# Optimization experiments

Measured on AMD Instinct MI355X. Metric: run time of the kernel, lower is better.

## Reference

```python
import jax, jax.numpy as jnp
import numpy as np

SCORE_THRESHOLD = 0.05
IOU_THRESHOLD = 0.5
MAX_DETECTIONS = 300
NEG = -1e9  # sentinel for suppressed / below-threshold scores


def setup_inputs() -> dict:
    key = jax.random.key(0)
    k1, k2, k3, k4 = jax.random.split(key, 4)
    B, N, C = 8, 49104, 20
    # valid corner-format boxes [x1, y1, x2, y2] inside a 512x512 image
    ctr = jax.random.uniform(k1, (B, N, 2), minval=0.0, maxval=512.0)
    wh = jax.random.uniform(k2, (B, N, 2), minval=8.0, maxval=128.0)
    boxes = jnp.concatenate([ctr - wh / 2, ctr + wh / 2], axis=-1)
    boxes3D = jax.random.normal(k3, (B, N, 16), dtype=jnp.float32)
    classification = jax.random.uniform(k4, (B, N, C)) ** 2
    return {"boxes": boxes, "boxes3D": boxes3D, "classification": classification}


def _iou_one_vs_all(box, boxes, areas):
    # box [4], boxes [N,4], areas [N] -> iou [N]
    lt = jnp.maximum(box[:2], boxes[:, :2])
    rb = jnp.minimum(box[2:], boxes[:, 2:])
    wh = jnp.maximum(rb - lt, 0.0)
    inter = wh[:, 0] * wh[:, 1]
    area = (box[2] - box[0]) * (box[3] - box[1])
    return inter / (areas + area - inter + 1e-9)


def _nms_class(boxes, areas, scores):
    # greedy NMS for one class; fixed MAX_DETECTIONS iterations (jit-friendly)
    s0 = jnp.where(scores > SCORE_THRESHOLD, scores, NEG)
    n = scores.shape[0]
    arange_n = jnp.arange(n)

    def step(s, _):
        i = jnp.argmax(s)
        valid = s[i] > NEG / 2
        iou = _iou_one_vs_all(boxes[i], boxes, areas)
        sup = (iou > IOU_THRESHOLD) | (arange_n == i)
        s_new = jnp.where(valid & sup, NEG, s)
        return s_new, (i, jnp.where(valid, s[i], NEG))

    _, (idx, sel) = jax.lax.scan(step, s0, None, length=MAX_DETECTIONS)
    return idx, sel  # [MAX_DETECTIONS] each


def _filter_image(boxes, boxes3D, cls):
    # boxes [N,4], boxes3D [N,16], cls [N,C]
    areas = (boxes[:, 2] - boxes[:, 0]) * (boxes[:, 3] - boxes[:, 1])
    # per-class NMS, vectorized over classes
    idxs, scs = jax.vmap(lambda s: _nms_class(boxes, areas, s), in_axes=1)(cls)  # [C, MAX]
    C = cls.shape[1]
    labels = jnp.broadcast_to(jnp.arange(C)[:, None], idxs.shape)
    # global top-k across all class candidates (invalid ones carry NEG score)
    top_sc, top_i = jax.lax.top_k(scs.reshape(-1), MAX_DETECTIONS)
    sel_anchor = idxs.reshape(-1)[top_i]
    sel_lab = labels.reshape(-1)[top_i]
    ok = top_sc > NEG / 2
    out_boxes = jnp.where(ok[:, None], boxes[sel_anchor], -1.0)
    out_b3d = jnp.where(ok[:, None], boxes3D[sel_anchor], -1.0)
    out_sc = jnp.where(ok, top_sc, -1.0)
    out_lab = jnp.where(ok, sel_lab, -1).astype(jnp.int32)
    return out_boxes, out_b3d, out_sc, out_lab


def reference(boxes, boxes3D, classification):
    # map over batch, like backend.map_fn in the original
    return jax.vmap(_filter_image)(boxes, boxes3D, classification)
```

## Files before the change

kernel.cpp:

```cpp
#include <hip/hip_runtime.h>

#define NCLS    20
#define NB      8
#define MAXDET  300
#define NEGV    (-1e9f)
#define NEGH    (-5e8f)
#define BLKN    512
#define BLKC    1024
#define KTARGET 448
#define KMAX    512
#define NBIN    256
#define NSLICE  64
#define SLSH    6
#define CSTR    16

#define T_MID   0x1.000001p-1

typedef unsigned long long u64;
typedef unsigned int u32;

__device__ __forceinline__ u64 packkey(float s, int j) {
    return ((u64)(__float_as_uint(s) ^ 0x80000000u) << 32) | (u32)(~(u32)j);
}
__device__ __forceinline__ u64 wredmax64(u64 k) {
#pragma unroll
    for (int off = 32; off > 0; off >>= 1) {
        u64 o = __shfl_xor(k, off);
        if (o > k) k = o;
    }
    return k;
}
__device__ __forceinline__ int binfull(float s) {
    int full = (int)(s * 262144.0f);
    return full > 262143 ? 262143 : full;
}
__device__ __forceinline__ int bin256(float s) { return binfull(s) >> 10; }

__global__ __launch_bounds__(256) void zero_kernel(u32* __restrict__ p, int nwords)
{
    int i = blockIdx.x * 256 + threadIdx.x;
    if (i < nwords) p[i] = 0;
}

__global__ __launch_bounds__(BLKN) void hist_kernel(
    const float* __restrict__ cls, u32* __restrict__ hist_slice_g, u32* __restrict__ hist_sum_g, int n)
{
    const int b = blockIdx.x & 7;
    const int slice = blockIdx.x >> 3;
    const int tid = threadIdx.x;
    const int F4 = (n * NCLS) >> 2;
    const int s0 = (int)(((long)slice * F4) >> SLSH);
    const int s1 = (int)(((long)(slice + 1) * F4) >> SLSH);

    __shared__ u32 lh[NCLS * NBIN];
    for (int i = tid; i < NCLS * NBIN; i += BLKN) lh[i] = 0;
    __syncthreads();

    const float4* p4 = (const float4*)(cls + (long)b * n * NCLS);
    for (int q = s0 + tid; q < s1; q += BLKN) {
        float4 v = p4[q];
        int f = q << 2;
        float ss[4] = {v.x, v.y, v.z, v.w};
#pragma unroll
        for (int e = 0; e < 4; ++e) {
            float sc = ss[e];
            if (sc > 0.05f) {
                u32 c = (u32)(f + e) % NCLS;
                atomicAdd(&lh[c * NBIN + bin256(sc)], 1u);
            }
        }
    }
    __syncthreads();
    u32* dst = hist_slice_g + (long)(b * NSLICE + slice) * (NCLS * NBIN);
    for (int i = tid; i < NCLS * NBIN; i += BLKN) {
        u32 v = lh[i];
        dst[i] = v;
        if (v) atomicAdd(&hist_sum_g[(b * NCLS + (i >> 8)) * NBIN + (i & 255)], v);
    }
}

__global__ __launch_bounds__(BLKN) void collect_kernel(
    const float* __restrict__ cls, const u32* __restrict__ hist_sum_g,
    const u32* __restrict__ hist_slice_g,
    u64* __restrict__ keys_g, u32* __restrict__ cntHi, u32* __restrict__ cntLo,
    int4* __restrict__ meta_g, int n)
{
    const int b = blockIdx.x & 7;
    const int slice = blockIdx.x >> 3;
    const int tid = threadIdx.x;
    const int lane = tid & 63;
    const int wv = tid >> 6;

    __shared__ u32 sumh[NCLS * NBIN];
    __shared__ int thrB[NCLS];
    __shared__ int cAs[NCLS];
    __shared__ int tots[NCLS];
    __shared__ u32 lcHi[NCLS], lcLo[NCLS], baseHi[NCLS], baseLo[NCLS];

    for (int i = tid; i < NCLS * NBIN; i += BLKN) sumh[i] = hist_sum_g[b * (NCLS * NBIN) + i];
    __syncthreads();

    for (int c = wv; c < NCLS; c += 8) {
        u32 h0 = sumh[c * NBIN + 4 * lane],     h1 = sumh[c * NBIN + 4 * lane + 1],
            h2 = sumh[c * NBIN + 4 * lane + 2], h3 = sumh[c * NBIN + 4 * lane + 3];
        int acc = (int)(h0 + h1 + h2 + h3);
#pragma unroll
        for (int d = 1; d < 64; d <<= 1) { int o = __shfl_down(acc, d); if (lane + d < 64) acc += o; }
        int S0 = acc, S1 = S0 - (int)h0, S2 = S1 - (int)h1, S3 = S2 - (int)h2, S4 = S3 - (int)h3;
        if (lane == 0) { thrB[c] = -1; cAs[c] = 0; tots[c] = S0; }
        int bin = -1, ca = 0;
        if      (S0 >= KTARGET && S1 < KTARGET) { bin = 4 * lane;     ca = S1; }
        else if (S1 >= KTARGET && S2 < KTARGET) { bin = 4 * lane + 1; ca = S2; }
        else if (S2 >= KTARGET && S3 < KTARGET) { bin = 4 * lane + 2; ca = S3; }
        else if (S3 >= KTARGET && S4 < KTARGET) { bin = 4 * lane + 3; ca = S4; }
        if (bin >= 0) { thrB[c] = bin; cAs[c] = ca; }
    }
    __syncthreads();

    if (slice == 0 && tid < NCLS) {
        meta_g[b * NCLS + tid] = make_int4(thrB[tid], cAs[tid], tots[tid], 0);
    }

    const u32* myh = hist_slice_g + (long)(b * NSLICE + slice) * (NCLS * NBIN);
    for (int c = wv; c < NCLS; c += 8) {
        const int B = thrB[c];
        u32 h0 = myh[c * NBIN + 4 * lane],     h1 = myh[c * NBIN + 4 * lane + 1],
            h2 = myh[c * NBIN + 4 * lane + 2], h3 = myh[c * NBIN + 4 * lane + 3];
        const int bin0 = 4 * lane;
        u32 part = 0;
        if (bin0     > B) part += h0;
        if (bin0 + 1 > B) part += h1;
        if (bin0 + 2 > B) part += h2;
        if (bin0 + 3 > B) part += h3;
        u32 lov = 0;
        if (B >= 0 && (B >> 2) == lane) lov = (B & 3) == 0 ? h0 : (B & 3) == 1 ? h1 : (B & 3) == 2 ? h2 : h3;
#pragma unroll
        for (int off = 32; off > 0; off >>= 1) {
            part += __shfl_xor(part, off);
            lov  += __shfl_xor(lov,  off);
        }
        if (lane == 0) { lcHi[c] = part; lcLo[c] = lov; }
    }
    __syncthreads();

    if (tid < NCLS) {
        const int pair = b * NCLS + tid;
        u32 h = lcHi[tid], l = lcLo[tid];
        baseHi[tid] = h ? atomicAdd(&cntHi[pair * CSTR], h) : 0u;
        baseLo[tid] = l ? atomicAdd(&cntLo[pair * CSTR], l) : 0u;
        lcHi[tid] = 0; lcLo[tid] = 0;
    }
    __syncthreads();

    const int F4 = (n * NCLS) >> 2;
    const int s0 = (int)(((long)slice * F4) >> SLSH);
    const int s1 = (int)(((long)(slice + 1) * F4) >> SLSH);
    const float4* p4 = (const float4*)(cls + (long)b * n * NCLS);
    for (int q = s0 + tid; q < s1; q += BLKN) {
        float4 v = p4[q];
        int f = q << 2;
        float ss[4] = {v.x, v.y, v.z, v.w};
#pragma unroll
        for (int e = 0; e < 4; ++e) {
            float sc = ss[e];
            if (sc > 0.05f) {
                u32 fe = (u32)(f + e);
                u32 c = fe % NCLS;
                int row = (int)(fe / NCLS);
                int bn = bin256(sc), B = thrB[c];
                const int pair = b * NCLS + (int)c;
                if (bn > B) {
                    u32 r = atomicAdd(&lcHi[c], 1u);
                    keys_g[(long)pair * KMAX + baseHi[c] + r] = packkey(sc, row);
                } else if (bn == B) {
                    u32 r = atomicAdd(&lcLo[c], 1u);
                    int pos = KMAX - 1 - (int)(baseLo[c] + r);
                    if (pos >= cAs[c]) keys_g[(long)pair * KMAX + pos] = packkey(sc, row);
                }
            }
        }
    }
}

__device__ __forceinline__ u64 cmb(u64 e, u64 p, int i, int jj, int k2) {
    bool up = ((i & k2) == 0);
    bool low = ((i & jj) == 0);
    return (up == low) ? (e > p ? e : p) : (e < p ? e : p);
}
__device__ __forceinline__ void sort512_1(u64& e, int tid, u64* bufA, u64* bufB) {
    int parity = 0;
    for (int k2 = 2; k2 <= KMAX; k2 <<= 1) {
        for (int jj = k2 >> 1; jj > 0; jj >>= 1) {
            if (jj >= 64) {
                u64* buf = parity ? bufB : bufA; parity ^= 1;
                if (tid < KMAX) buf[tid] = e;
                __syncthreads();
                if (tid < KMAX) { u64 p = buf[tid ^ jj]; e = cmb(e, p, tid, jj, k2); }
            } else {
                if (tid < KMAX) { u64 p = __shfl_xor(e, jj); e = cmb(e, p, tid, jj, k2); }
            }
        }
    }
    __syncthreads();
    if (tid < KMAX) bufA[tid] = e;
    __syncthreads();
}

template<bool PRE>
__global__ __launch_bounds__(BLKC, 1) void nms_final_kernel(
    const float4* __restrict__ boxes,
    const float*  __restrict__ cls,
    const u64* __restrict__ keys_g,
    const int4* __restrict__ meta_g,
    const u32* __restrict__ cntHi_g, const u32* __restrict__ cntLo_g,
    float* __restrict__ sel_ws, int* __restrict__ idx_ws, int n)
{
    const int b = blockIdx.x & 7;
    const int c = blockIdx.x >> 3;
    const int pair = b * NCLS + c;
    const int tid = threadIdx.x;
    const int lane = tid & 63;
    const int wv = tid >> 6;

    const float4* bb = boxes + (long)b * n;
    const float* srow = cls + (long)b * n * NCLS + c;
    float* selp = sel_ws + pair * MAXDET;
    int*   idxp = idx_ws + pair * MAXDET;

    __shared__ u64    keysA[KMAX], keysB[KMAX];
    __shared__ float4 cbox[KMAX];
    __shared__ float4 aBox[MAXDET];
    __shared__ u32    hist256[NBIN];
    __shared__ u32    kb0[64], kb1[64], psupm[2];
    __shared__ u64    wl[16];
    __shared__ int    ctrl[8];
    __shared__ u64    ubk;

    if (tid == 0) { ubk = ~0ull; ctrl[5] = 0; }
    if (tid < 64) { kb0[tid] = 0; kb1[tid] = 0; }
    if (tid < 2)  psupm[tid] = 0;
    bool first = true;
    __syncthreads();

    while (true) {
        const u64 UB = ubk;
        u64 e = 0;
        int trusted, cumTotal, cumAbove;

        if (PRE && first) {
            const int4 m = meta_g[pair];
            cumTotal = m.z;
            if (cumTotal == 0) break;
            cumAbove = m.y;
            const int hi = (int)cntHi_g[pair * CSTR];
            const int lo = (int)cntLo_g[pair * CSTR];
            const bool dropped = lo > (KMAX - cumAbove);
            trusted = dropped ? cumAbove : (hi + lo);
            const int lo_start = dropped ? cumAbove : (KMAX - lo);
            if (tid < KMAX && (tid < hi || tid >= lo_start)) e = keys_g[(long)pair * KMAX + tid];
            if (trusted > 0) {
                sort512_1(e, tid, keysA, keysB);
            } else {
                u64 lb = 0;
                for (int j = tid; j < n; j += BLKC) {
                    float sc = srow[(long)j * NCLS];
                    if (sc > 0.05f) { u64 ky = packkey(sc, j); if (ky < UB && ky > lb) lb = ky; }
                }
                lb = wredmax64(lb);
                if (lane == 0) wl[wv] = lb;
                __syncthreads();
                if (tid == 0) { u64 bk = 0; for (int w = 0; w < 16; ++w) if (wl[w] > bk) bk = wl[w]; keysA[0] = bk; }
                trusted = 1;
                __syncthreads();
            }
        } else {
            if (tid < NBIN) hist256[tid] = 0;
            if (tid < KMAX) keysA[tid] = 0;
            if (tid > 0 && tid < 5) ctrl[tid] = 0;
            if (tid == 0) ctrl[0] = -1;
            __syncthreads();
            for (int j = tid; j < n; j += BLKC) {
                float sc = srow[(long)j * NCLS];
                if (sc > 0.05f) { u64 ky = packkey(sc, j); if (ky < UB) atomicAdd(&hist256[bin256(sc)], 1u); }
            }
            __syncthreads();
            if (wv == 0) {
                u32 h0 = hist256[4 * lane], h1 = hist256[4 * lane + 1],
                    h2 = hist256[4 * lane + 2], h3 = hist256[4 * lane + 3];
                int acc = (int)(h0 + h1 + h2 + h3);
#pragma unroll
                for (int d = 1; d < 64; d <<= 1) { int o = __shfl_down(acc, d); if (lane + d < 64) acc += o; }
                int S0 = acc, S1 = S0 - (int)h0, S2 = S1 - (int)h1, S3 = S2 - (int)h2, S4 = S3 - (int)h3;
                if (lane == 0) { ctrl[0] = -1; ctrl[1] = 0; ctrl[2] = S0; }
                int bin = -1, ca = 0;
                if      (S0 >= KTARGET && S1 < KTARGET) { bin = 4 * lane;     ca = S1; }
                else if (S1 >= KTARGET && S2 < KTARGET) { bin = 4 * lane + 1; ca = S2; }
                else if (S2 >= KTARGET && S3 < KTARGET) { bin = 4 * lane + 2; ca = S3; }
                else if (S3 >= KTARGET && S4 < KTARGET) { bin = 4 * lane + 3; ca = S4; }
                if (bin >= 0) { ctrl[0] = bin; ctrl[1] = ca; }
            }
            __syncthreads();
            cumTotal = ctrl[2];
            if (cumTotal == 0) break;
            cumAbove = ctrl[1];
            const int B = ctrl[0];
            for (int j = tid; j < n; j += BLKC) {
                float sc = srow[(long)j * NCLS];
                if (sc > 0.05f) {
                    u64 ky = packkey(sc, j);
                    if (ky < UB) {
                        int bn = bin256(sc);
                        if (bn > B) { int sl = atomicAdd(&ctrl[4], 1); if (sl < KMAX) keysA[sl] = ky; }
                        else if (bn == B) {
                            int p = atomicAdd(&ctrl[3], 1);
                            int pos = KMAX - 1 - p;
                            if (pos >= cumAbove) keysA[pos] = ky;
                        }
                    }
                }
            }
            __syncthreads();
            const int cLo = ctrl[3], cHi = ctrl[4];
            const bool dropped = (cHi + cLo) > KMAX;
            trusted = dropped ? cHi : (cHi + cLo);
            if (trusted > 0) {
                if (tid < KMAX) e = keysA[tid];
                __syncthreads();
                sort512_1(e, tid, keysA, keysB);
            } else {
                u64 lb = 0;
                for (int j = tid; j < n; j += BLKC) {
                    float sc = srow[(long)j * NCLS];
                    if (sc > 0.05f) { u64 ky = packkey(sc, j); if (ky < UB && ky > lb) lb = ky; }
                }
                lb = wredmax64(lb);
                if (lane == 0) wl[wv] = lb;
                __syncthreads();
                if (tid == 0) { u64 bk = 0; for (int w = 0; w < 16; ++w) if (wl[w] > bk) bk = wl[w]; keysA[0] = bk; }
                trusted = 1;
                __syncthreads();
            }
        }

        if (tid < KMAX) {
            u64 ky = (tid < trusted) ? keysA[tid] : 0;
            float4 bx = make_float4(0.f, 0.f, 0.f, 0.f);
            if (tid < trusted) bx = bb[(int)(~(u32)ky)];
            cbox[tid] = bx;
        }
        __syncthreads();

        for (int base = 0; base < trusted; base += 64) {
            const int kcur = ctrl[5];
            if (kcur >= MAXDET) break;
            const int ci = base + lane;
            const bool have = ci < trusted;
            const float4 pb = cbox[have ? ci : 0];
            const float par = (pb.z - pb.x) * (pb.w - pb.y);

            bool sup = false;
            for (int a = wv; a < kcur; a += 16) {
                float4 ab = aBox[a];
                float am = (ab.z - ab.x) * (ab.w - ab.y);
                float ltx = fmaxf(ab.x, pb.x), lty = fmaxf(ab.y, pb.y);
                float rbx = fminf(ab.z, pb.z), rby = fminf(ab.w, pb.w);
                float wx = fmaxf(rbx - ltx, 0.0f), wy = fmaxf(rby - lty, 0.0f);
                float inter = wx * wy;
                float den = ((par + am) - inter) + 1e-9f;
                sup = sup || ((double)inter > T_MID * (double)den);
            }
            u64 bal = __ballot(sup && have);
            if (lane == 0 && bal) { atomicOr(&psupm[0], (u32)bal); atomicOr(&psupm[1], (u32)(bal >> 32)); }

#pragma unroll
            for (int r = 0; r < 4; ++r) {
                const int m = (r << 4) | wv;
                if (lane < m && (base + m) < trusted) {
                    float4 vb = cbox[base + m];
                    float va = (vb.z - vb.x) * (vb.w - vb.y);
                    float ltx = fmaxf(pb.x, vb.x), lty = fmaxf(pb.y, vb.y);
                    float rbx = fminf(pb.z, vb.z), rby = fminf(pb.w, vb.w);
                    float wx = fmaxf(rbx - ltx, 0.0f), wy = fmaxf(rby - lty, 0.0f);
                    float inter = wx * wy;
                    float den = ((va + par) - inter) + 1e-9f;
                    if ((double)inter > T_MID * (double)den) {
                        if (lane < 32) atomicOr(&kb0[m], 1u << lane);
                        else           atomicOr(&kb1[m], 1u << (lane - 32));
                    }
                }
            }
            __syncthreads();

            if (tid < 64) {
                const u64 kbm = ((u64)kb1[lane] << 32) | kb0[lane];
                const u64 ps  = ((u64)psupm[1] << 32) | psupm[0];
                const bool alive0 = have && !((ps >> lane) & 1);
                u64 accm = __ballot(alive0);
                for (int it = 0; it < 64; ++it) {
                    u64 nm = __ballot(alive0 && ((kbm & accm) == 0ull));
                    if (nm == accm) break;
                    accm = nm;
                }
                const bool a = (accm >> lane) & 1;
                const int rank = (int)__popcll(accm & ((1ull << lane) - 1ull));
                const int rem = MAXDET - kcur;
                if (a && rank < rem) {
                    const int slot = kcur + rank;
                    aBox[slot] = pb;
                    const u64 ky = keysA[ci];
                    selp[slot] = __uint_as_float((u32)(ky >> 32) ^ 0x80000000u);
                    idxp[slot] = (int)(~(u32)ky);
                }
                kb0[lane] = 0; kb1[lane] = 0;
                if (lane < 2) psupm[lane] = 0;
                if (lane == 0) {
                    const int cnt = (int)__popcll(accm);
                    ctrl[5] = kcur + (cnt < rem ? cnt : rem);
                }
            }
            __syncthreads();
        }

        if (tid == 0) ubk = keysA[trusted - 1];
        first = false;
        __syncthreads();
        if (ctrl[5] >= MAXDET || cumTotal - trusted <= 0) break;
    }

    const int kfin = ctrl[5];
    for (int f = kfin + tid; f < MAXDET; f += BLKC) { selp[f] = NEGV; idxp[f] = 0; }
}

#define OFF_B3D (NB * MAXDET * 4)
#define OFF_SC  (OFF_B3D + NB * MAXDET * 16)
#define OFF_LAB (OFF_SC + NB * MAXDET)

__global__ __launch_bounds__(1024, 1) void topk_kernel(
    const float4* __restrict__ boxes,
    const float*  __restrict__ b3d,
    const float*  __restrict__ sel_ws,
    const int*    __restrict__ idx_ws,
    float* __restrict__ out,
    int n)
{
    const int b = blockIdx.x;
    const int tid = threadIdx.x;
    const int lane = tid & 63;
    const int wv = tid >> 6;
    const int M = NCLS * MAXDET;

    __shared__ u64  kall[NCLS * MAXDET];
    __shared__ u32  h1[512];
    __shared__ u64  keysA[512], keysB[512];
    __shared__ int  wts[8], ews[8];
    __shared__ int  ctrl[8];
    __shared__ int  outA[MAXDET];

    const float* sp = sel_ws + b * M;
    for (int f = tid; f < M; f += 1024) {
        float v = sp[f];
        kall[f] = (v > 0.05f) ? packkey(v, f) : 0ull;
    }
    if (tid < 512) { h1[tid] = 0; keysA[tid] = 0; }
    if (tid > 0 && tid < 8) ctrl[tid] = 0;
    if (tid == 0) { ctrl[0] = -1; ctrl[5] = -1; }
    __syncthreads();

    for (int f = tid; f < M; f += 1024) {
        u64 k = kall[f];
        if (k) {
            float s = __uint_as_float((u32)(k >> 32) ^ 0x80000000u);
            atomicAdd(&h1[binfull(s) >> 9], 1u);
        }
    }
    __syncthreads();
    {
        const int h = (tid < 512) ? (int)h1[tid] : 0;
        int acc = h;
#pragma unroll
        for (int d = 1; d < 64; d <<= 1) { int o = __shfl_down(acc, d); if (lane + d < 64) acc += o; }
        if (lane == 0 && wv < 8) wts[wv] = acc;
        __syncthreads();
        if (tid < 8) { int e = 0; for (int w = tid + 1; w < 8; ++w) e += wts[w]; ews[tid] = e; }
        __syncthreads();
        if (tid < 512) {
            const int S = acc + ews[wv];
            if (S >= MAXDET && (S - h) < MAXDET) { ctrl[0] = tid; ctrl[1] = S - h; }
            if (tid == 0) ctrl[2] = S;
        }
    }
    __syncthreads();
    const int B1 = ctrl[0];
    const int cA1 = ctrl[1];

    if (tid < 512) h1[tid] = 0;
    __syncthreads();
    if (B1 >= 0) {
        for (int f = tid; f < M; f += 1024) {
            u64 k = kall[f];
            if (k) {
                float s = __uint_as_float((u32)(k >> 32) ^ 0x80000000u);
                int full = binfull(s);
                if ((full >> 9) == B1) atomicAdd(&h1[full & 511], 1u);
            }
        }
    }
    __syncthreads();
    const int KT2 = MAXDET - cA1;
    {
        const int h = (tid < 512) ? (int)h1[tid] : 0;
        int acc = h;
#pragma unroll
        for (int d = 1; d < 64; d <<= 1) { int o = __shfl_down(acc, d); if (lane + d < 64) acc += o; }
        if (lane == 0 && wv < 8) wts[wv] = acc;
        __syncthreads();
        if (tid < 8) { int e = 0; for (int w = tid + 1; w < 8; ++w) e += wts[w]; ews[tid] = e; }
        __syncthreads();
        if (tid < 512) {
            const int S = acc + ews[wv];
            if (B1 >= 0 && S >= KT2 && (S - h) < KT2) { ctrl[5] = tid; ctrl[6] = S - h; }
        }
    }
    __syncthreads();
    const int B2 = ctrl[5];
    const int cA2 = ctrl[6];

    for (int f = tid; f < M; f += 1024) {
        u64 k = kall[f];
        if (k) {
            float s = __uint_as_float((u32)(k >> 32) ^ 0x80000000u);
            int full = binfull(s);
            int bkt = full >> 9, sub = full & 511;
            bool hi = (B1 < 0) || (bkt > B1) || (bkt == B1 && sub > B2);
            bool lo = (B1 >= 0) && (bkt == B1) && (sub == B2);
            if (hi) { int slot = atomicAdd(&ctrl[3], 1); if (slot < 512) keysA[slot] = k; }
            else if (lo) { int p = atomicAdd(&ctrl[4], 1); int pos = 511 - p; if (pos >= cA1 + cA2) keysA[pos] = k; }
        }
    }
    __syncthreads();
    const bool dropped = (ctrl[3] + ctrl[4]) > 512;

    if (!dropped) {
        u64 e = (tid < 512) ? keysA[tid] : 0;
        int parity = 0;
        for (int k2 = 2; k2 <= 512; k2 <<= 1) {
            for (int jj = k2 >> 1; jj > 0; jj >>= 1) {
                if (jj >= 64) {
                    u64* buf = parity ? keysB : keysA; parity ^= 1;
                    if (tid < 512) buf[tid] = e;
                    __syncthreads();
                    if (tid < 512) { u64 p = buf[tid ^ jj]; e = cmb(e, p, tid, jj, k2); }
                } else {
                    if (tid < 512) { u64 p = __shfl_xor(e, jj); e = cmb(e, p, tid, jj, k2); }
                }
            }
        }
        __syncthreads();
        if (tid < 512) keysA[tid] = e;
        __syncthreads();
    } else {
        if (tid < 64) {
            int pos = 0;
            for (int k = 0; k < MAXDET; ++k) {
                u64 key = 0;
                if (lane < NCLS && pos < MAXDET) key = kall[lane * MAXDET + pos];
                u64 r = wredmax64(key);
                if (r != 0) {
                    u64 bal = __ballot(key == r);
                    int w = __ffsll((long long)bal) - 1;
                    if (lane == w) pos++;
                }
                if (lane == 0) keysA[k] = r;
            }
        }
        __syncthreads();
    }

    for (int k = tid; k < MAXDET; k += 1024) {
        const u64 kk = keysA[k];
        const bool ok = kk != 0;
        const int flat = (int)(~(u32)kk);
        const float sc = __uint_as_float((u32)(kk >> 32) ^ 0x80000000u);
        const int a = ok ? idx_ws[b * M + flat] : -1;
        const int cc = flat / MAXDET;
        float4 bx = make_float4(-1.f, -1.f, -1.f, -1.f);
        if (ok) bx = boxes[(long)b * n + a];
        out[(long)b * MAXDET * 4 + k * 4 + 0] = bx.x;
        out[(long)b * MAXDET * 4 + k * 4 + 1] = bx.y;
        out[(long)b * MAXDET * 4 + k * 4 + 2] = bx.z;
        out[(long)b * MAXDET * 4 + k * 4 + 3] = bx.w;
        out[OFF_SC  + (long)b * MAXDET + k] = ok ? sc : -1.0f;
        out[OFF_LAB + (long)b * MAXDET + k] = ok ? (float)cc : -1.0f;
        outA[k] = a;
    }
    __syncthreads();
    for (int q = tid; q < MAXDET * 16; q += 1024) {
        const int k = q >> 4;
        const int a = outA[k];
        out[OFF_B3D + (long)b * MAXDET * 16 + q] = (a >= 0) ? b3d[((long)b * n + a) * 16 + (q & 15)] : -1.0f;
    }
}

extern "C" void kernel_launch(void* const* d_in, const int* in_sizes, int n_in,
                              void* d_out, int out_size, void* d_ws, size_t ws_size,
                              hipStream_t stream)
{
    const float* boxes = (const float*)d_in[0];
    const float* b3d   = (const float*)d_in[1];
    const float* cls   = (const float*)d_in[2];
    float* out = (float*)d_out;

    const int n = in_sizes[0] / (NB * 4);
    const int NP = NB * NCLS;

    const size_t sumB   = (size_t)NP * NBIN * sizeof(u32);
    const size_t cntB   = (size_t)NP * CSTR * sizeof(u32);
    const size_t metaB  = (size_t)NP * sizeof(int4);
    const size_t sliceB = (size_t)NB * NSLICE * NCLS * NBIN * sizeof(u32);
    const size_t keysB_ = (size_t)NP * KMAX * sizeof(u64);
    const size_t selB   = (size_t)NP * MAXDET * sizeof(float);

    char* p = (char*)d_ws;
    u32*  hist_sum_g   = (u32*)p;          p += sumB;
    u32*  cntHi        = (u32*)p;          p += cntB;
    u32*  cntLo        = (u32*)p;          p += cntB;
    int4* meta_g       = (int4*)p;         p += metaB;
    u32*  hist_slice_g = (u32*)p;          p += sliceB;
    u64*  keys_g       = (u64*)p;          p += keysB_;
    float* sel_ws      = (float*)p;        p += selB;
    int*   idx_ws      = (int*)p;          p += selB;

    if (ws_size >= (size_t)(p - (char*)d_ws)) {
        const int zwords = (int)((sumB + 2 * cntB) / sizeof(u32));
        hipLaunchKernelGGL(zero_kernel, dim3((zwords + 255) / 256), dim3(256), 0, stream,
                           hist_sum_g, zwords);
        hipLaunchKernelGGL(hist_kernel, dim3(NB * NSLICE), dim3(BLKN), 0, stream,
                           cls, hist_slice_g, hist_sum_g, n);
        hipLaunchKernelGGL(collect_kernel, dim3(NB * NSLICE), dim3(BLKN), 0, stream,
                           cls, hist_sum_g, hist_slice_g, keys_g, cntHi, cntLo, meta_g, n);
        hipLaunchKernelGGL((nms_final_kernel<true>), dim3(NP), dim3(BLKC), 0, stream,
                           (const float4*)boxes, cls, keys_g, meta_g, cntHi, cntLo,
                           sel_ws, idx_ws, n);
        hipLaunchKernelGGL(topk_kernel, dim3(NB), dim3(1024), 0, stream,
                           (const float4*)boxes, b3d, sel_ws, idx_ws, out, n);
    } else {
        float* sel2 = (float*)d_ws;
        int*   idx2 = (int*)((char*)d_ws + selB);
        hipLaunchKernelGGL((nms_final_kernel<false>), dim3(NP), dim3(BLKC), 0, stream,
                           (const float4*)boxes, cls, nullptr, nullptr, nullptr, nullptr,
                           sel2, idx2, n);
        hipLaunchKernelGGL(topk_kernel, dim3(NB), dim3(1024), 0, stream,
                           (const float4*)boxes, b3d, sel2, idx2, out, n);
    }
}
```

Baseline: 93.34 us.

## Replace histogram-based candidate selection with fixed-threshold segmented collection

Drops the histogram pass and the adaptive bin threshold. The collect kernel now gathers every score above a fixed constant into per-pair, per-segment buckets of capacity 128, using global atomic counters. The NMS kernel sorts up to 1024 prefetched keys with a full-block bitonic sort, and falls back to the full scan path when a segment overflows or is empty. This removes one full read of the classification tensor and one kernel launch, but the constant is tuned to the score distribution and the sort is now twice as large.

```diff
diff --git a/kernel.cpp b/kernel.cpp
--- a/kernel.cpp
+++ b/kernel.cpp
@@ -7,12 +7,15 @@
 #define NEGH    (-5e8f)
 #define BLKN    512
 #define BLKC    1024
-#define KTARGET 448
-#define KMAX    512
+#define KTARGET 896
+#define KMAX    1024
 #define NBIN    256
 #define NSLICE  64
 #define SLSH    6
+#define NSEG    8
+#define SEGCAP  128
 #define CSTR    16
+#define T0F     0.97974f
 
 #define T_MID   0x1.000001p-1
 
@@ -42,19 +45,16 @@
     if (i < nwords) p[i] = 0;
 }
 
-__global__ __launch_bounds__(BLKN) void hist_kernel(
-    const float* __restrict__ cls, u32* __restrict__ hist_slice_g, u32* __restrict__ hist_sum_g, int n)
+__global__ __launch_bounds__(BLKN) void collect_kernel(
+    const float* __restrict__ cls, u64* __restrict__ keys_g, u32* __restrict__ cnt_g, int n)
 {
     const int b = blockIdx.x & 7;
     const int slice = blockIdx.x >> 3;
+    const int seg = slice >> 3;
     const int tid = threadIdx.x;
     const int F4 = (n * NCLS) >> 2;
     const int s0 = (int)(((long)slice * F4) >> SLSH);
     const int s1 = (int)(((long)(slice + 1) * F4) >> SLSH);
-
-    __shared__ u32 lh[NCLS * NBIN];
-    for (int i = tid; i < NCLS * NBIN; i += BLKN) lh[i] = 0;
-    __syncthreads();
 
     const float4* p4 = (const float4*)(cls + (long)b * n * NCLS);
     for (int q = s0 + tid; q < s1; q += BLKN) {
@@ -64,119 +64,14 @@
 #pragma unroll
         for (int e = 0; e < 4; ++e) {
             float sc = ss[e];
-            if (sc > 0.05f) {
-                u32 c = (u32)(f + e) % NCLS;
-                atomicAdd(&lh[c * NBIN + bin256(sc)], 1u);
-            }
-        }
-    }
-    __syncthreads();
-    u32* dst = hist_slice_g + (long)(b * NSLICE + slice) * (NCLS * NBIN);
-    for (int i = tid; i < NCLS * NBIN; i += BLKN) {
-        u32 v = lh[i];
-        dst[i] = v;
-        if (v) atomicAdd(&hist_sum_g[(b * NCLS + (i >> 8)) * NBIN + (i & 255)], v);
-    }
-}
-
-__global__ __launch_bounds__(BLKN) void collect_kernel(
-    const float* __restrict__ cls, const u32* __restrict__ hist_sum_g,
-    const u32* __restrict__ hist_slice_g,
-    u64* __restrict__ keys_g, u32* __restrict__ cntHi, u32* __restrict__ cntLo,
-    int4* __restrict__ meta_g, int n)
-{
-    const int b = blockIdx.x & 7;
-    const int slice = blockIdx.x >> 3;
-    const int tid = threadIdx.x;
-    const int lane = tid & 63;
-    const int wv = tid >> 6;
-
-    __shared__ u32 sumh[NCLS * NBIN];
-    __shared__ int thrB[NCLS];
-    __shared__ int cAs[NCLS];
-    __shared__ int tots[NCLS];
-    __shared__ u32 lcHi[NCLS], lcLo[NCLS], baseHi[NCLS], baseLo[NCLS];
-
-    for (int i = tid; i < NCLS * NBIN; i += BLKN) sumh[i] = hist_sum_g[b * (NCLS * NBIN) + i];
-    __syncthreads();
-
-    for (int c = wv; c < NCLS; c += 8) {
-        u32 h0 = sumh[c * NBIN + 4 * lane],     h1 = sumh[c * NBIN + 4 * lane + 1],
-            h2 = sumh[c * NBIN + 4 * lane + 2], h3 = sumh[c * NBIN + 4 * lane + 3];
-        int acc = (int)(h0 + h1 + h2 + h3);
-#pragma unroll
-        for (int d = 1; d < 64; d <<= 1) { int o = __shfl_down(acc, d); if (lane + d < 64) acc += o; }
-        int S0 = acc, S1 = S0 - (int)h0, S2 = S1 - (int)h1, S3 = S2 - (int)h2, S4 = S3 - (int)h3;
-        if (lane == 0) { thrB[c] = -1; cAs[c] = 0; tots[c] = S0; }
-        int bin = -1, ca = 0;
-        if      (S0 >= KTARGET && S1 < KTARGET) { bin = 4 * lane;     ca = S1; }
-        else if (S1 >= KTARGET && S2 < KTARGET) { bin = 4 * lane + 1; ca = S2; }
-        else if (S2 >= KTARGET && S3 < KTARGET) { bin = 4 * lane + 2; ca = S3; }
-        else if (S3 >= KTARGET && S4 < KTARGET) { bin = 4 * lane + 3; ca = S4; }
-        if (bin >= 0) { thrB[c] = bin; cAs[c] = ca; }
-    }
-    __syncthreads();
-
-    if (slice == 0 && tid < NCLS) {
-        meta_g[b * NCLS + tid] = make_int4(thrB[tid], cAs[tid], tots[tid], 0);
-    }
-
-    const u32* myh = hist_slice_g + (long)(b * NSLICE + slice) * (NCLS * NBIN);
-    for (int c = wv; c < NCLS; c += 8) {
-        const int B = thrB[c];
-        u32 h0 = myh[c * NBIN + 4 * lane],     h1 = myh[c * NBIN + 4 * lane + 1],
-            h2 = myh[c * NBIN + 4 * lane + 2], h3 = myh[c * NBIN + 4 * lane + 3];
-        const int bin0 = 4 * lane;
-        u32 part = 0;
-        if (bin0     > B) part += h0;
-        if (bin0 + 1 > B) part += h1;
-        if (bin0 + 2 > B) part += h2;
-        if (bin0 + 3 > B) part += h3;
-        u32 lov = 0;
-        if (B >= 0 && (B >> 2) == lane) lov = (B & 3) == 0 ? h0 : (B & 3) == 1 ? h1 : (B & 3) == 2 ? h2 : h3;
-#pragma unroll
-        for (int off = 32; off > 0; off >>= 1) {
-            part += __shfl_xor(part, off);
-            lov  += __shfl_xor(lov,  off);
-        }
-        if (lane == 0) { lcHi[c] = part; lcLo[c] = lov; }
-    }
-    __syncthreads();
-
-    if (tid < NCLS) {
-        const int pair = b * NCLS + tid;
-        u32 h = lcHi[tid], l = lcLo[tid];
-        baseHi[tid] = h ? atomicAdd(&cntHi[pair * CSTR], h) : 0u;
-        baseLo[tid] = l ? atomicAdd(&cntLo[pair * CSTR], l) : 0u;
-        lcHi[tid] = 0; lcLo[tid] = 0;
-    }
-    __syncthreads();
-
-    const int F4 = (n * NCLS) >> 2;
-    const int s0 = (int)(((long)slice * F4) >> SLSH);
-    const int s1 = (int)(((long)(slice + 1) * F4) >> SLSH);
-    const float4* p4 = (const float4*)(cls + (long)b * n * NCLS);
-    for (int q = s0 + tid; q < s1; q += BLKN) {
-        float4 v = p4[q];
-        int f = q << 2;
-        float ss[4] = {v.x, v.y, v.z, v.w};
-#pragma unroll
-        for (int e = 0; e < 4; ++e) {
-            float sc = ss[e];
-            if (sc > 0.05f) {
+            if (sc > T0F) {
                 u32 fe = (u32)(f + e);
                 u32 c = fe % NCLS;
                 int row = (int)(fe / NCLS);
-                int bn = bin256(sc), B = thrB[c];
                 const int pair = b * NCLS + (int)c;
-                if (bn > B) {
-                    u32 r = atomicAdd(&lcHi[c], 1u);
-                    keys_g[(long)pair * KMAX + baseHi[c] + r] = packkey(sc, row);
-                } else if (bn == B) {
-                    u32 r = atomicAdd(&lcLo[c], 1u);
-                    int pos = KMAX - 1 - (int)(baseLo[c] + r);
-                    if (pos >= cAs[c]) keys_g[(long)pair * KMAX + pos] = packkey(sc, row);
-                }
+                u32 slot = atomicAdd(&cnt_g[(pair * NSEG + seg) * CSTR], 1u);
+                if (slot < SEGCAP)
+                    keys_g[(long)pair * KMAX + (seg << 7) + slot] = packkey(sc, row);
             }
         }
     }
@@ -187,22 +82,24 @@
     bool low = ((i & jj) == 0);
     return (up == low) ? (e > p ? e : p) : (e < p ? e : p);
 }
-__device__ __forceinline__ void sort512_1(u64& e, int tid, u64* bufA, u64* bufB) {
+__device__ __forceinline__ void sort1024_1(u64& e, int tid, u64* bufA, u64* bufB) {
     int parity = 0;
     for (int k2 = 2; k2 <= KMAX; k2 <<= 1) {
         for (int jj = k2 >> 1; jj > 0; jj >>= 1) {
             if (jj >= 64) {
                 u64* buf = parity ? bufB : bufA; parity ^= 1;
-                if (tid < KMAX) buf[tid] = e;
+                buf[tid] = e;
                 __syncthreads();
-                if (tid < KMAX) { u64 p = buf[tid ^ jj]; e = cmb(e, p, tid, jj, k2); }
+                u64 p = buf[tid ^ jj];
+                e = cmb(e, p, tid, jj, k2);
             } else {
-                if (tid < KMAX) { u64 p = __shfl_xor(e, jj); e = cmb(e, p, tid, jj, k2); }
-            }
-        }
-    }
-    __syncthreads();
-    if (tid < KMAX) bufA[tid] = e;
+                u64 p = __shfl_xor(e, jj);
+                e = cmb(e, p, tid, jj, k2);
+            }
+        }
+    }
+    __syncthreads();
+    bufA[tid] = e;
     __syncthreads();
 }
 
@@ -211,8 +108,7 @@
     const float4* __restrict__ boxes,
     const float*  __restrict__ cls,
     const u64* __restrict__ keys_g,
-    const int4* __restrict__ meta_g,
-    const u32* __restrict__ cntHi_g, const u32* __restrict__ cntLo_g,
+    const u32* __restrict__ cnt_g,
     float* __restrict__ sel_ws, int* __restrict__ idx_ws, int n)
 {
     const int b = blockIdx.x & 7;
@@ -236,6 +132,19 @@
     __shared__ int    ctrl[8];
     __shared__ u64    ubk;
 
+    int pre_tot = 0; bool pre_ok = false; int my_cnt = 0;
+    if (PRE) {
+        bool over = false;
+#pragma unroll
+        for (int s = 0; s < NSEG; ++s) {
+            int cv = (int)cnt_g[(pair * NSEG + s) * CSTR];
+            pre_tot += cv;
+            over = over || (cv > SEGCAP);
+        }
+        pre_ok = (!over) && (pre_tot > 0);
+        my_cnt = (int)cnt_g[(pair * NSEG + (tid >> 7)) * CSTR];
+    }
+
     if (tid == 0) { ubk = ~0ull; ctrl[5] = 0; }
     if (tid < 64) { kb0[tid] = 0; kb1[tid] = 0; }
     if (tid < 2)  psupm[tid] = 0;
@@ -245,37 +154,16 @@
     while (true) {
         const u64 UB = ubk;
         u64 e = 0;
-        int trusted, cumTotal, cumAbove;
-
-        if (PRE && first) {
-            const int4 m = meta_g[pair];
-            cumTotal = m.z;
-            if (cumTotal == 0) break;
-            cumAbove = m.y;
-            const int hi = (int)cntHi_g[pair * CSTR];
-            const int lo = (int)cntLo_g[pair * CSTR];
-            const bool dropped = lo > (KMAX - cumAbove);
-            trusted = dropped ? cumAbove : (hi + lo);
-            const int lo_start = dropped ? cumAbove : (KMAX - lo);
-            if (tid < KMAX && (tid < hi || tid >= lo_start)) e = keys_g[(long)pair * KMAX + tid];
-            if (trusted > 0) {
-                sort512_1(e, tid, keysA, keysB);
-            } else {
-                u64 lb = 0;
-                for (int j = tid; j < n; j += BLKC) {
-                    float sc = srow[(long)j * NCLS];
-                    if (sc > 0.05f) { u64 ky = packkey(sc, j); if (ky < UB && ky > lb) lb = ky; }
-                }
-                lb = wredmax64(lb);
-                if (lane == 0) wl[wv] = lb;
-                __syncthreads();
-                if (tid == 0) { u64 bk = 0; for (int w = 0; w < 16; ++w) if (wl[w] > bk) bk = wl[w]; keysA[0] = bk; }
-                trusted = 1;
-                __syncthreads();
-            }
+        int trusted, cumTotal;
+
+        if (PRE && first && pre_ok) {
+            cumTotal = 0x7fffffff;
+            trusted = pre_tot;
+            if ((tid & (SEGCAP - 1)) < my_cnt) e = keys_g[(long)pair * KMAX + tid];
+            sort1024_1(e, tid, keysA, keysB);
         } else {
             if (tid < NBIN) hist256[tid] = 0;
-            if (tid < KMAX) keysA[tid] = 0;
+            keysA[tid] = 0;
             if (tid > 0 && tid < 5) ctrl[tid] = 0;
             if (tid == 0) ctrl[0] = -1;
             __syncthreads();
@@ -302,7 +190,7 @@
             __syncthreads();
             cumTotal = ctrl[2];
             if (cumTotal == 0) break;
-            cumAbove = ctrl[1];
+            const int cumAbove = ctrl[1];
             const int B = ctrl[0];
             for (int j = tid; j < n; j += BLKC) {
                 float sc = srow[(long)j * NCLS];
@@ -324,9 +212,9 @@
             const bool dropped = (cHi + cLo) > KMAX;
             trusted = dropped ? cHi : (cHi + cLo);
             if (trusted > 0) {
-                if (tid < KMAX) e = keysA[tid];
+                e = keysA[tid];
                 __syncthreads();
-                sort512_1(e, tid, keysA, keysB);
+                sort1024_1(e, tid, keysA, keysB);
             } else {
                 u64 lb = 0;
                 for (int j = tid; j < n; j += BLKC) {
@@ -342,7 +230,7 @@
             }
         }
 
-        if (tid < KMAX) {
+        {
             u64 ky = (tid < trusted) ? keysA[tid] : 0;
             float4 bx = make_float4(0.f, 0.f, 0.f, 0.f);
             if (tid < trusted) bx = bb[(int)(~(u32)ky)];
@@ -613,42 +501,31 @@
     const int n = in_sizes[0] / (NB * 4);
     const int NP = NB * NCLS;
 
-    const size_t sumB   = (size_t)NP * NBIN * sizeof(u32);
-    const size_t cntB   = (size_t)NP * CSTR * sizeof(u32);
-    const size_t metaB  = (size_t)NP * sizeof(int4);
-    const size_t sliceB = (size_t)NB * NSLICE * NCLS * NBIN * sizeof(u32);
+    const size_t cntB   = (size_t)NP * NSEG * CSTR * sizeof(u32);
     const size_t keysB_ = (size_t)NP * KMAX * sizeof(u64);
     const size_t selB   = (size_t)NP * MAXDET * sizeof(float);
 
     char* p = (char*)d_ws;
-    u32*  hist_sum_g   = (u32*)p;          p += sumB;
-    u32*  cntHi        = (u32*)p;          p += cntB;
-    u32*  cntLo        = (u32*)p;          p += cntB;
-    int4* meta_g       = (int4*)p;         p += metaB;
-    u32*  hist_slice_g = (u32*)p;          p += sliceB;
-    u64*  keys_g       = (u64*)p;          p += keysB_;
-    float* sel_ws      = (float*)p;        p += selB;
-    int*   idx_ws      = (int*)p;          p += selB;
+    u32*  cnt_g  = (u32*)p;                p += cntB;
+    u64*  keys_g = (u64*)p;                p += keysB_;
+    float* sel_ws = (float*)p;             p += selB;
+    int*   idx_ws = (int*)p;               p += selB;
 
     if (ws_size >= (size_t)(p - (char*)d_ws)) {
-        const int zwords = (int)((sumB + 2 * cntB) / sizeof(u32));
+        const int zwords = (int)(cntB / sizeof(u32));
         hipLaunchKernelGGL(zero_kernel, dim3((zwords + 255) / 256), dim3(256), 0, stream,
-                           hist_sum_g, zwords);
-        hipLaunchKernelGGL(hist_kernel, dim3(NB * NSLICE), dim3(BLKN), 0, stream,
-                           cls, hist_slice_g, hist_sum_g, n);
+                           cnt_g, zwords);
         hipLaunchKernelGGL(collect_kernel, dim3(NB * NSLICE), dim3(BLKN), 0, stream,
-                           cls, hist_sum_g, hist_slice_g, keys_g, cntHi, cntLo, meta_g, n);
+                           cls, keys_g, cnt_g, n);
         hipLaunchKernelGGL((nms_final_kernel<true>), dim3(NP), dim3(BLKC), 0, stream,
-                           (const float4*)boxes, cls, keys_g, meta_g, cntHi, cntLo,
-                           sel_ws, idx_ws, n);
+                           (const float4*)boxes, cls, keys_g, cnt_g, sel_ws, idx_ws, n);
         hipLaunchKernelGGL(topk_kernel, dim3(NB), dim3(1024), 0, stream,
                            (const float4*)boxes, b3d, sel_ws, idx_ws, out, n);
     } else {
         float* sel2 = (float*)d_ws;
         int*   idx2 = (int*)((char*)d_ws + selB);
         hipLaunchKernelGGL((nms_final_kernel<false>), dim3(NP), dim3(BLKC), 0, stream,
-                           (const float4*)boxes, cls, nullptr, nullptr, nullptr, nullptr,
-                           sel2, idx2, n);
+                           (const float4*)boxes, cls, nullptr, nullptr, sel2, idx2, n);
         hipLaunchKernelGGL(topk_kernel, dim3(NB), dim3(1024), 0, stream,
                            (const float4*)boxes, b3d, sel2, idx2, out, n);
     }
```

After: 77.64 us. 16.8% less time.
